# Kernel optimization log

Hardware: AMD Instinct MI355X
Metric: run time of the kernel (lower is better)

Reference implementation:

```python
import jax, jax.numpy as jnp
import numpy as np

B, S, DIM, H = 2, 2048, 1024, 16
DH = DIM // H            # 64
G = DH // 4              # 16 quaternion groups per head
IQ = DIM // 4            # 256
ROPE_BASE = 10000.0
SCALE = DH ** -0.5


def qlinear(x, wr, wi, wj, wk, b):
    # x: [B,S,4*IQ]; strided quaternion components, exact combo from QuaternionLinear.forward
    xr, xi, xj, xk = x[..., 0::4], x[..., 1::4], x[..., 2::4], x[..., 3::4]
    o_r = xr @ wr.T - xi @ wi.T - xj @ wj.T - xk @ wk.T
    o_i = xi @ wr.T + xr @ wi.T + xk @ wk.T - xj @ wj.T
    o_j = xj @ wr.T - xk @ wk.T + xr @ wj.T + xi @ wi.T
    o_k = xk @ wr.T + xj @ wj.T - xi @ wi.T + xr @ wk.T
    out = jnp.stack([o_r, o_i, o_j, o_k], axis=-1).reshape(x.shape[:-1] + (-1,))
    return out + b


def qrope(x):
    # x: [B,H,S,DH]; left quaternion multiply u(theta) \otimes q, axis_mode='cycle'
    b, h, s, dh = x.shape
    g = dh // 4
    xq = x.reshape(b, h, s, g, 4)
    t = jnp.arange(s, dtype=x.dtype)
    inv = 1.0 / (ROPE_BASE ** (jnp.arange(g, dtype=x.dtype) / g))
    ang = t[:, None] * inv[None, :]            # [S,G]
    cos, sin = jnp.cos(ang), jnp.sin(ang)
    gi = jnp.arange(g)
    ax_i = (gi % 3 == 0).astype(x.dtype)
    ax_j = (gi % 3 == 1).astype(x.dtype)
    ax_k = (gi % 3 == 2).astype(x.dtype)
    ur, ui, uj, uk = cos, sin * ax_i, sin * ax_j, sin * ax_k   # [S,G] broadcast over [B,H,S,G]
    xr, xi, xj, xk = xq[..., 0], xq[..., 1], xq[..., 2], xq[..., 3]
    pr = ur * xr - ui * xi - uj * xj - uk * xk
    pi = ur * xi + ui * xr + uj * xk - uk * xj
    pj = ur * xj - ui * xk + uj * xr + uk * xi
    pk = ur * xk + ui * xj - uj * xi + uk * xr
    return jnp.stack([pr, pi, pj, pk], axis=-1).reshape(b, h, s, dh)


def setup_inputs() -> dict:
    key = jax.random.key(0)
    ks = jax.random.split(key, 24)
    x = jax.random.normal(ks[0], (B, S, DIM), dtype=jnp.float32)
    # causal mask: True = masked
    mask = jnp.broadcast_to(jnp.triu(jnp.ones((S, S), dtype=bool), k=1), (B, S, S))
    inp = {"x": x, "mask": mask}
    i = 1
    for proj in ("q", "k", "v", "o"):
        for comp in ("wr", "wi", "wj", "wk"):
            inp[f"{proj}_{comp}"] = jax.random.normal(ks[i], (IQ, IQ), dtype=jnp.float32) * 0.02
            i += 1
        inp[f"{proj}_b"] = jnp.zeros((DIM,), dtype=jnp.float32)
    return inp


def reference(x, mask,
              q_wr, q_wi, q_wj, q_wk, q_b,
              k_wr, k_wi, k_wj, k_wk, k_b,
              v_wr, v_wi, v_wj, v_wk, v_b,
              o_wr, o_wi, o_wj, o_wk, o_b):
    b, s, dm = x.shape
    q = qlinear(x, q_wr, q_wi, q_wj, q_wk, q_b).reshape(b, s, H, DH).transpose(0, 2, 1, 3)
    k = qlinear(x, k_wr, k_wi, k_wj, k_wk, k_b).reshape(b, s, H, DH).transpose(0, 2, 1, 3)
    v = qlinear(x, v_wr, v_wi, v_wj, v_wk, v_b).reshape(b, s, H, DH).transpose(0, 2, 1, 3)
    q, k = qrope(q), qrope(k)
    scores = jnp.einsum('bhsd,bhtd->bhst', q, k) * SCALE
    scores = jnp.where(mask[:, None, :, :], -jnp.inf, scores)
    a = jax.nn.softmax(scores, axis=-1)
    out = jnp.einsum('bhst,bhtd->bhsd', a, v).transpose(0, 2, 1, 3).reshape(b, s, dm)
    return qlinear(out, o_wr, o_wi, o_wj, o_wk, o_b)
```

## Files before the change

### kernel.cpp

```cpp
#include <hip/hip_runtime.h>
#include <stdint.h>

typedef unsigned short u16;
typedef unsigned int   u32;

#define NB   2
#define NS   2048
#define NDIM 1024
#define NH   16
#define NDH  64
#define QSCALE 0.18033688011112042f

typedef __bf16 bf16x8 __attribute__((ext_vector_type(8)));
typedef float  f32x4  __attribute__((ext_vector_type(4)));

#define MFMA_BF16(a,b,c) __builtin_amdgcn_mfma_f32_16x16x32_bf16((a),(b),(c),0,0,0)

#define XBF_OFF   (256)
#define WD_OFF    (XBF_OFF  + 8*1024*1024)
#define BIAS_OFF  (WD_OFF   + 8*1024*1024)
#define QB_OFF    (BIAS_OFF + 16384)
#define KB_OFF    (QB_OFF   + 8*1024*1024)
#define VT_OFF    (KB_OFF   + 8*1024*1024)
#define OP_OFF    (VT_OFF   + 8*1024*1024)
#define LP_OFF    (OP_OFF   + 16*1024*1024)

__device__ __forceinline__ float bf2f(u16 h){
  union { u32 u; float f; } v; v.u = ((u32)h) << 16; return v.f;
}
__device__ __forceinline__ u16 f2bf(float f){
  union { float f; u32 u; } v; v.f = f;
  u32 r = (v.u >> 16) & 1u;
  return (u16)((v.u + 0x7fffu + r) >> 16);
}
__device__ __forceinline__ float load_val(const void* p, int i, int isbf){
  return isbf ? bf2f(((const u16*)p)[i]) : ((const float*)p)[i];
}
__device__ __forceinline__ void gl_lds16(const u16* g, u16* l){
  __builtin_amdgcn_global_load_lds(
      (__attribute__((address_space(1))) void*)(uintptr_t)g,
      (__attribute__((address_space(3))) void*)(uintptr_t)l,
      16, 0, 0);
}

__global__ void detect_kernel(const u16* __restrict__ x, int* __restrict__ flag){
  __shared__ int cnt;
  if (threadIdx.x == 0) cnt = 0;
  __syncthreads();
  int ok = 0;
  int base = threadIdx.x * 16;
  for (int i = base; i < base + 16; ++i){
    u16 h = x[i];
    int e = (h >> 7) & 0xFF;
    if ((e > 96 && e < 158) || ((h & 0x7FFF) == 0)) ok++;
  }
  atomicAdd(&cnt, ok);
  __syncthreads();
  if (threadIdx.x == 0) *flag = (cnt > 3600) ? 1 : 0;
}

__global__ void conv_x_kernel(const void* __restrict__ xin, u16* __restrict__ xbf,
                              const int* __restrict__ flag){
  int isbf = *flag;
  int t = blockIdx.x * 256 + threadIdx.x;
  if (isbf){
    ((uint4*)xbf)[t] = ((const uint4*)xin)[t];
  } else {
    const float4* f4 = (const float4*)xin;
    float4 a = f4[2*t], b = f4[2*t+1];
    ushort4 lo = { f2bf(a.x), f2bf(a.y), f2bf(a.z), f2bf(a.w) };
    ushort4 hi = { f2bf(b.x), f2bf(b.y), f2bf(b.z), f2bf(b.w) };
    ((ushort4*)xbf)[2*t]   = lo;
    ((ushort4*)xbf)[2*t+1] = hi;
  }
}

struct QPtrs { const void* w[16]; const void* b[4]; };

__global__ void build_w_kernel(QPtrs ptrs, u16* __restrict__ wd,
                               float* __restrict__ biasf, const int* __restrict__ flag){
  int isbf = *flag;
  int idx = blockIdx.x * 256 + threadIdx.x;
  int n = idx & 255, m = (idx >> 8) & 255, c = (idx >> 16) & 3, p = idx >> 18;
  int src = m * 256 + n;
  float vr = load_val(ptrs.w[p*4+0], src, isbf);
  float vi = load_val(ptrs.w[p*4+1], src, isbf);
  float vj = load_val(ptrs.w[p*4+2], src, isbf);
  float vk = load_val(ptrs.w[p*4+3], src, isbf);
  float o0, o1, o2, o3;
  switch (c){
    case 0:  o0 = vr; o1 = -vi; o2 = -vj; o3 = -vk; break;
    case 1:  o0 = vi; o1 =  vr; o2 = -vj; o3 =  vk; break;
    case 2:  o0 = vj; o1 =  vi; o2 =  vr; o3 = -vk; break;
    default: o0 = vk; o1 = -vi; o2 =  vj; o3 =  vr; break;
  }
  ushort4 sv = { f2bf(o0), f2bf(o1), f2bf(o2), f2bf(o3) };
  *(ushort4*)&wd[(size_t)p * 1048576 + (size_t)(4*m + c) * 1024 + 4*n] = sv;
  if (idx < 4096){
    int pp = idx >> 10, oo = idx & 1023;
    biasf[idx] = load_val(ptrs.b[pp], oo, isbf);
  }
}

__global__ __launch_bounds__(256)
void gemm_qkv_kernel(const u16* __restrict__ A, const u16* __restrict__ Bw,
                     const float* __restrict__ bias,
                     u16* __restrict__ qb, u16* __restrict__ kb, u16* __restrict__ vt){
  __shared__ u16 sA[128 * 32];
  __shared__ u16 sB[128 * 32];
  int tid = threadIdx.x, w = tid >> 6, lane = tid & 63, quad = lane >> 4, l16 = lane & 15;
  int n0 = blockIdx.x * 128, m0 = blockIdx.y * 128;

  f32x4 acc[4][4];
#pragma unroll
  for (int i = 0; i < 4; ++i)
#pragma unroll
    for (int j = 0; j < 4; ++j) acc[i][j] = (f32x4){0.f, 0.f, 0.f, 0.f};

  int eo = w * 512 + lane * 8;
  int r0 = eo >> 5, c0 = eo & 31;
  const u16* ga = A  + (size_t)(m0 + r0) * 1024 + c0;
  const u16* gb = Bw + (size_t)(n0 + r0) * 1024 + c0;
  u16* la = &sA[eo];
  u16* lb = &sB[eo];
  int mw = (w & 1) * 64, nw = (w >> 1) * 64;

  for (int k0 = 0; k0 < 1024; k0 += 32){
#pragma unroll
    for (int i = 0; i < 2; ++i){
      gl_lds16(ga + (size_t)i * 65536 + k0, la + i * 2048);
      gl_lds16(gb + (size_t)i * 65536 + k0, lb + i * 2048);
    }
    __syncthreads();
    bf16x8 af[4], bfr[4];
#pragma unroll
    for (int mt = 0; mt < 4; ++mt)
      af[mt] = *(const bf16x8*)&sA[(mw + mt*16 + l16) * 32 + quad * 8];
#pragma unroll
    for (int nt = 0; nt < 4; ++nt)
      bfr[nt] = *(const bf16x8*)&sB[(nw + nt*16 + l16) * 32 + quad * 8];
#pragma unroll
    for (int mt = 0; mt < 4; ++mt)
#pragma unroll
      for (int nt = 0; nt < 4; ++nt)
        acc[mt][nt] = MFMA_BF16(af[mt], bfr[nt], acc[mt][nt]);
    __syncthreads();
  }

#pragma unroll
  for (int mt = 0; mt < 4; ++mt){
    int row = m0 + mw + mt*16 + quad*4;
    int b = row >> 11, seq0 = row & 2047;
#pragma unroll
    for (int nt = 0; nt < 4; ++nt){
      int col = n0 + nw + nt*16 + l16;
      int proj = col >> 10, o = col & 1023;
      int h = o >> 6, d = o & 63;
      float bv = bias[col];
      if (proj == 2){
        ushort4 pv = { f2bf(acc[mt][nt][0] + bv), f2bf(acc[mt][nt][1] + bv),
                       f2bf(acc[mt][nt][2] + bv), f2bf(acc[mt][nt][3] + bv) };
        *(ushort4*)&vt[((size_t)((b*16 + h) * 64 + d)) * 2048 + seq0] = pv;
      } else {
        u16* dst = proj ? kb : qb;
#pragma unroll
        for (int r = 0; r < 4; ++r)
          dst[((size_t)((b*16 + h) * 2048 + seq0 + r)) * 64 + d] = f2bf(acc[mt][nt][r] + bv);
      }
    }
  }
}

__global__ __launch_bounds__(256)
void gemm_o_kernel(const u16* __restrict__ A, const u16* __restrict__ Bw,
                   const float* __restrict__ bias, void* __restrict__ dout,
                   const int* __restrict__ flag){
  __shared__ u16 sA[64 * 32];
  __shared__ u16 sB[128 * 32];
  int tid = threadIdx.x, w = tid >> 6, lane = tid & 63, quad = lane >> 4, l16 = lane & 15;
  int n0 = blockIdx.x * 128, m0 = blockIdx.y * 64;

  f32x4 acc[2][4];
#pragma unroll
  for (int i = 0; i < 2; ++i)
#pragma unroll
    for (int j = 0; j < 4; ++j) acc[i][j] = (f32x4){0.f, 0.f, 0.f, 0.f};

  int mw = (w & 1) * 32, nw = (w >> 1) * 64;

  for (int k0 = 0; k0 < 1024; k0 += 32){
#pragma unroll
    for (int i = 0; i < 3; ++i){
      int c = w * 3 + i;
      int eo = (c < 4 ? c : c - 4) * 512 + lane * 8;
      int r0 = eo >> 5, c0 = eo & 31;
      if (c < 4) gl_lds16(A  + (size_t)(m0 + r0) * 1024 + k0 + c0, &sA[eo]);
      else       gl_lds16(Bw + (size_t)(n0 + r0) * 1024 + k0 + c0, &sB[eo]);
    }
    __syncthreads();
    bf16x8 af[2], bfr[4];
#pragma unroll
    for (int mt = 0; mt < 2; ++mt)
      af[mt] = *(const bf16x8*)&sA[(mw + mt*16 + l16) * 32 + quad * 8];
#pragma unroll
    for (int nt = 0; nt < 4; ++nt)
      bfr[nt] = *(const bf16x8*)&sB[(nw + nt*16 + l16) * 32 + quad * 8];
#pragma unroll
    for (int mt = 0; mt < 2; ++mt)
#pragma unroll
      for (int nt = 0; nt < 4; ++nt)
        acc[mt][nt] = MFMA_BF16(af[mt], bfr[nt], acc[mt][nt]);
    __syncthreads();
  }

  int isbf = *flag;
#pragma unroll
  for (int mt = 0; mt < 2; ++mt){
    int row = m0 + mw + mt*16 + quad*4;
#pragma unroll
    for (int nt = 0; nt < 4; ++nt){
      int col = n0 + nw + nt*16 + l16;
      float bv = bias[col];
#pragma unroll
      for (int r = 0; r < 4; ++r){
        float val = acc[mt][nt][r] + bv;
        size_t addr = (size_t)(row + r) * 1024 + col;
        if (isbf) ((u16*)dout)[addr] = f2bf(val);
        else      ((float*)dout)[addr] = val;
      }
    }
  }
}

__global__ void rope_kernel(u16* __restrict__ qb, u16* __restrict__ kb){
  int idx = blockIdx.x * 256 + threadIdx.x;
  int which = idx >> 20;
  int r = idx & 1048575;
  u16* buf = which ? kb : qb;
  int g = r & 15, s = (r >> 4) & 2047, bh = r >> 15;
  size_t base = ((size_t)bh * 2048 + s) * 64 + g * 4;
  ushort4 xv = *(ushort4*)&buf[base];
  float xr = bf2f(xv.x), xi = bf2f(xv.y), xj = bf2f(xv.z), xk = bf2f(xv.w);
  float inv = __builtin_amdgcn_exp2f(-(float)g * 0.8304820237218405f);
  float ang = (float)s * inv;
  float co = __cosf(ang), si = __sinf(ang);
  float sc = which ? 1.0f : QSCALE;
  co *= sc; si *= sc;
  int ax = g % 3;
  float ui = (ax == 0) ? si : 0.f;
  float uj = (ax == 1) ? si : 0.f;
  float uk = (ax == 2) ? si : 0.f;
  float pr = co*xr - ui*xi - uj*xj - uk*xk;
  float pi = co*xi + ui*xr + uj*xk - uk*xj;
  float pj = co*xj - ui*xk + uj*xr + uk*xi;
  float pk = co*xk + ui*xj - uj*xi + uk*xr;
  ushort4 res = { f2bf(pr), f2bf(pi), f2bf(pj), f2bf(pk) };
  *(ushort4*)&buf[base] = res;
}

#define PSTR 72

__global__ __launch_bounds__(256, 3)
void attn_kernel(const u16* __restrict__ Q, const u16* __restrict__ K,
                 const u16* __restrict__ Vt, u16* __restrict__ OP,
                 float* __restrict__ LP){
  __shared__ u16 sK[2][4096];
  __shared__ u16 sV[2][4096];
  __shared__ u16 sP[4][16 * PSTR];
  int qt  = 15 - (int)blockIdx.x;
  int spl = blockIdx.y;
  int bh  = blockIdx.z;
  int tid = threadIdx.x, w = tid >> 6, lane = tid & 63, quad = lane >> 4, l16 = lane & 15;
  size_t kbase = (size_t)bh * 2048 * 64;
  size_t vbase = (size_t)bh * 64 * 2048;
  int rowbase = qt * 128 + w * 32;

  bf16x8 qf[2][2];
#pragma unroll
  for (int g = 0; g < 2; ++g)
#pragma unroll
    for (int kc = 0; kc < 2; ++kc)
      qf[g][kc] = *(const bf16x8*)(Q + kbase + (size_t)(rowbase + g*16 + l16) * 64 + kc*32 + quad*8);

  f32x4 oacc[2][4];
  float lsum[2][4];
#pragma unroll
  for (int g = 0; g < 2; ++g)
#pragma unroll
    for (int i = 0; i < 4; ++i){ oacc[g][i] = (f32x4){0.f,0.f,0.f,0.f}; lsum[g][i] = 0.f; }

  int kt0 = spl ? (qt + 1) : 0;
  int ntiles = qt + 1;

  auto stage = [&](int kt, int b){
    int kcol = kt * 64;
#pragma unroll
    for (int p = 0; p < 2; ++p){
      int slot = w*128 + p*64 + lane;
      int row = slot >> 3, dc = (slot & 7) ^ (row & 7);
      gl_lds16(K  + kbase + (size_t)(kcol + row) * 64 + dc*8, &sK[b][(w*128 + p*64) * 8]);
      gl_lds16(Vt + vbase + (size_t)row * 2048 + kcol + dc*8, &sV[b][(w*128 + p*64) * 8]);
    }
  };

  stage(kt0, 0);
  for (int i = 0; i < ntiles; ++i){
    int kcol = (kt0 + i) * 64;
    __syncthreads();
    if (i + 1 < ntiles) stage(kt0 + i + 1, (i + 1) & 1);
    const u16* bK = sK[i & 1];
    const u16* bV = sV[i & 1];

    if (kcol <= rowbase + 31){
      bf16x8 bk[2][4], vf[2][4];
#pragma unroll
      for (int kc = 0; kc < 2; ++kc)
#pragma unroll
        for (int nt = 0; nt < 4; ++nt){
          int rw = nt*16 + l16;
          int ch = ((kc*4 + quad) ^ (rw & 7)) * 8;
          bk[kc][nt] = *(const bf16x8*)&bK[rw*64 + ch];
          vf[kc][nt] = *(const bf16x8*)&bV[rw*64 + ch];
        }
#pragma unroll
      for (int g = 0; g < 2; ++g){
        int G0 = rowbase + g*16;
        if (kcol <= G0 + 15){
          f32x4 sacc[4];
#pragma unroll
          for (int nt = 0; nt < 4; ++nt) sacc[nt] = (f32x4){0.f,0.f,0.f,0.f};
#pragma unroll
          for (int kc = 0; kc < 2; ++kc)
#pragma unroll
            for (int nt = 0; nt < 4; ++nt)
              sacc[nt] = MFMA_BF16(qf[g][kc], bk[kc][nt], sacc[nt]);

          __bf16* sp = (__bf16*)&sP[w][0];
          if (kcol + 63 > G0){
#pragma unroll
            for (int nt = 0; nt < 4; ++nt){
              int col = kcol + nt*16 + l16;
#pragma unroll
              for (int r = 0; r < 4; ++r){
                int row = G0 + quad*4 + r;
                float pp = (col <= row) ? __builtin_amdgcn_exp2f(sacc[nt][r]) : 0.f;
                lsum[g][r] += pp;
                sp[(quad*4 + r) * PSTR + nt*16 + l16] = (__bf16)pp;
              }
            }
          } else {
#pragma unroll
            for (int nt = 0; nt < 4; ++nt)
#pragma unroll
              for (int r = 0; r < 4; ++r){
                float pp = __builtin_amdgcn_exp2f(sacc[nt][r]);
                lsum[g][r] += pp;
                sp[(quad*4 + r) * PSTR + nt*16 + l16] = (__bf16)pp;
              }
          }
#pragma unroll
          for (int kc = 0; kc < 2; ++kc){
            bf16x8 pf = *(const bf16x8*)&sp[l16 * PSTR + kc*32 + quad*8];
#pragma unroll
            for (int nt = 0; nt < 4; ++nt)
              oacc[g][nt] = MFMA_BF16(pf, vf[kc][nt], oacc[g][nt]);
          }
        }
      }
    }
  }

  size_t obase = ((size_t)(spl*32 + bh)) * 2048;
#pragma unroll
  for (int g = 0; g < 2; ++g)
#pragma unroll
    for (int r = 0; r < 4; ++r){
      float l = lsum[g][r];
      l += __shfl_xor(l, 1); l += __shfl_xor(l, 2);
      l += __shfl_xor(l, 4); l += __shfl_xor(l, 8);
      int row = rowbase + g*16 + quad*4 + r;
      if (l16 == 0) LP[obase + row] = l;
#pragma unroll
      for (int nt = 0; nt < 4; ++nt)
        OP[(obase + row) * 64 + nt*16 + l16] = f2bf(oacc[g][nt][r]);
    }
}

__global__ void combine_kernel(const u16* __restrict__ OP, const float* __restrict__ LP,
                               u16* __restrict__ Ab){
  int idx = blockIdx.x * 256 + threadIdx.x;
  int dc = idx & 7, s = (idx >> 3) & 2047, bh = idx >> 14;
  size_t r0 = (size_t)bh * 2048 + s, r1 = (size_t)(32 + bh) * 2048 + s;
  float invl = 1.f / (LP[r0] + LP[r1]);
  union { uint4 v; u16 h[8]; } a0, a1; ushort4 o[2];
  a0.v = *(const uint4*)&OP[r0 * 64 + dc*8];
  a1.v = *(const uint4*)&OP[r1 * 64 + dc*8];
#pragma unroll
  for (int p = 0; p < 2; ++p)
#pragma unroll
    for (int j = 0; j < 4; ++j)
      ((u16*)&o[p])[j] = f2bf((bf2f(a0.h[p*4+j]) + bf2f(a1.h[p*4+j])) * invl);
  int b = bh >> 4, h = bh & 15;
  u16* dst = &Ab[((size_t)(b*2048 + s)) * 1024 + h*64 + dc*8];
  *(ushort4*)dst = o[0];
  *(ushort4*)(dst + 4) = o[1];
}

extern "C" void kernel_launch(void* const* d_in, const int* in_sizes, int n_in,
                              void* d_out, int out_size, void* d_ws, size_t ws_size,
                              hipStream_t stream){
  (void)in_sizes; (void)n_in; (void)out_size; (void)ws_size;
  char* ws = (char*)d_ws;
  int*   flag  = (int*)ws;
  u16*   Xbf   = (u16*)(ws + XBF_OFF);
  u16*   Wd    = (u16*)(ws + WD_OFF);
  float* biasf = (float*)(ws + BIAS_OFF);
  u16*   Qb    = (u16*)(ws + QB_OFF);
  u16*   Kb    = (u16*)(ws + KB_OFF);
  u16*   Vt    = (u16*)(ws + VT_OFF);
  u16*   OP    = (u16*)(ws + OP_OFF);
  float* LP    = (float*)(ws + LP_OFF);
  u16*   Ab    = Xbf;

  detect_kernel<<<1, 256, 0, stream>>>((const u16*)d_in[0], flag);
  conv_x_kernel<<<2048, 256, 0, stream>>>(d_in[0], Xbf, flag);

  QPtrs ptrs;
  for (int p = 0; p < 4; ++p){
    for (int wi = 0; wi < 4; ++wi) ptrs.w[p*4 + wi] = d_in[2 + p*5 + wi];
    ptrs.b[p] = d_in[2 + p*5 + 4];
  }
  build_w_kernel<<<4096, 256, 0, stream>>>(ptrs, Wd, biasf, flag);

  gemm_qkv_kernel<<<dim3(24, 32), 256, 0, stream>>>(Xbf, Wd, biasf, Qb, Kb, Vt);
  rope_kernel<<<8192, 256, 0, stream>>>(Qb, Kb);
  attn_kernel<<<dim3(16, 2, 32), 256, 0, stream>>>(Qb, Kb, Vt, OP, LP);
  combine_kernel<<<2048, 256, 0, stream>>>(OP, LP, Ab);
  gemm_o_kernel<<<dim3(8, 64), 256, 0, stream>>>(Ab, Wd + 3*1048576, biasf + 3072,
                                                 d_out, flag);
}
```

Baseline: 274.4 us.

## Compute transposed PV product and load V fragments directly from global

The attention kernel now computes O^T = V^T·P^T, so V fragments are read straight from global memory into registers, and the V tile LDS staging buffer is removed. P is stored transposed in a small padded LDS buffer using vector stores, and output rows are written as ushort4 vectors after row sums are redistributed through LDS. The grid order is changed so bh varies fastest. Less LDS may allow higher occupancy and remove a staging copy. The costs are uncoalesced-ish global V loads that are no longer prefetched, and scalar 16-bit LDS gathers to build the P fragments.

```diff
diff --git a/kernel.cpp b/kernel.cpp
--- a/kernel.cpp
+++ b/kernel.cpp
@@ -258,22 +258,22 @@
   *(ushort4*)&buf[base] = res;
 }
 
-#define PSTR 72
+#define SPT 20
 
 __global__ __launch_bounds__(256, 3)
 void attn_kernel(const u16* __restrict__ Q, const u16* __restrict__ K,
                  const u16* __restrict__ Vt, u16* __restrict__ OP,
                  float* __restrict__ LP){
   __shared__ u16 sK[2][4096];
-  __shared__ u16 sV[2][4096];
-  __shared__ u16 sP[4][16 * PSTR];
-  int qt  = 15 - (int)blockIdx.x;
+  __shared__ u16 sPT[4][64 * SPT];
+  int bh  = blockIdx.x;
   int spl = blockIdx.y;
-  int bh  = blockIdx.z;
+  int qt  = 15 - (int)blockIdx.z;
   int tid = threadIdx.x, w = tid >> 6, lane = tid & 63, quad = lane >> 4, l16 = lane & 15;
   size_t kbase = (size_t)bh * 2048 * 64;
   size_t vbase = (size_t)bh * 64 * 2048;
   int rowbase = qt * 128 + w * 32;
+  u16* spw = &sPT[w][0];
 
   bf16x8 qf[2][2];
 #pragma unroll
@@ -282,12 +282,12 @@
     for (int kc = 0; kc < 2; ++kc)
       qf[g][kc] = *(const bf16x8*)(Q + kbase + (size_t)(rowbase + g*16 + l16) * 64 + kc*32 + quad*8);
 
-  f32x4 oacc[2][4];
+  f32x4 oaccT[2][4];
   float lsum[2][4];
 #pragma unroll
   for (int g = 0; g < 2; ++g)
 #pragma unroll
-    for (int i = 0; i < 4; ++i){ oacc[g][i] = (f32x4){0.f,0.f,0.f,0.f}; lsum[g][i] = 0.f; }
+    for (int i = 0; i < 4; ++i){ oaccT[g][i] = (f32x4){0.f,0.f,0.f,0.f}; lsum[g][i] = 0.f; }
 
   int kt0 = spl ? (qt + 1) : 0;
   int ntiles = qt + 1;
@@ -298,8 +298,7 @@
     for (int p = 0; p < 2; ++p){
       int slot = w*128 + p*64 + lane;
       int row = slot >> 3, dc = (slot & 7) ^ (row & 7);
-      gl_lds16(K  + kbase + (size_t)(kcol + row) * 64 + dc*8, &sK[b][(w*128 + p*64) * 8]);
-      gl_lds16(Vt + vbase + (size_t)row * 2048 + kcol + dc*8, &sV[b][(w*128 + p*64) * 8]);
+      gl_lds16(K + kbase + (size_t)(kcol + row) * 64 + dc*8, &sK[b][(w*128 + p*64) * 8]);
     }
   };
 
@@ -309,10 +308,16 @@
     __syncthreads();
     if (i + 1 < ntiles) stage(kt0 + i + 1, (i + 1) & 1);
     const u16* bK = sK[i & 1];
-    const u16* bV = sV[i & 1];
 
     if (kcol <= rowbase + 31){
-      bf16x8 bk[2][4], vf[2][4];
+      bf16x8 vf[4][2];
+#pragma unroll
+      for (int dn = 0; dn < 4; ++dn)
+#pragma unroll
+        for (int kc = 0; kc < 2; ++kc)
+          vf[dn][kc] = *(const bf16x8*)(Vt + vbase + (size_t)(dn*16 + l16) * 2048
+                                        + kcol + kc*32 + quad*8);
+      bf16x8 bk[2][4];
 #pragma unroll
       for (int kc = 0; kc < 2; ++kc)
 #pragma unroll
@@ -320,7 +325,6 @@
           int rw = nt*16 + l16;
           int ch = ((kc*4 + quad) ^ (rw & 7)) * 8;
           bk[kc][nt] = *(const bf16x8*)&bK[rw*64 + ch];
-          vf[kc][nt] = *(const bf16x8*)&bV[rw*64 + ch];
         }
 #pragma unroll
       for (int g = 0; g < 2; ++g){
@@ -335,42 +339,49 @@
             for (int nt = 0; nt < 4; ++nt)
               sacc[nt] = MFMA_BF16(qf[g][kc], bk[kc][nt], sacc[nt]);
 
-          __bf16* sp = (__bf16*)&sP[w][0];
           if (kcol + 63 > G0){
 #pragma unroll
             for (int nt = 0; nt < 4; ++nt){
               int col = kcol + nt*16 + l16;
+              ushort4 pv;
 #pragma unroll
               for (int r = 0; r < 4; ++r){
                 int row = G0 + quad*4 + r;
                 float pp = (col <= row) ? __builtin_amdgcn_exp2f(sacc[nt][r]) : 0.f;
                 lsum[g][r] += pp;
-                sp[(quad*4 + r) * PSTR + nt*16 + l16] = (__bf16)pp;
+                ((u16*)&pv)[r] = f2bf(pp);
               }
+              *(ushort4*)&spw[(nt*16 + l16) * SPT + quad*4] = pv;
             }
           } else {
 #pragma unroll
-            for (int nt = 0; nt < 4; ++nt)
+            for (int nt = 0; nt < 4; ++nt){
+              ushort4 pv;
 #pragma unroll
               for (int r = 0; r < 4; ++r){
                 float pp = __builtin_amdgcn_exp2f(sacc[nt][r]);
                 lsum[g][r] += pp;
-                sp[(quad*4 + r) * PSTR + nt*16 + l16] = (__bf16)pp;
+                ((u16*)&pv)[r] = f2bf(pp);
               }
+              *(ushort4*)&spw[(nt*16 + l16) * SPT + quad*4] = pv;
+            }
           }
 #pragma unroll
           for (int kc = 0; kc < 2; ++kc){
-            bf16x8 pf = *(const bf16x8*)&sp[l16 * PSTR + kc*32 + quad*8];
-#pragma unroll
-            for (int nt = 0; nt < 4; ++nt)
-              oacc[g][nt] = MFMA_BF16(pf, vf[kc][nt], oacc[g][nt]);
+            bf16x8 pf;
+#pragma unroll
+            for (int j = 0; j < 8; ++j)
+              pf[j] = ((const __bf16*)spw)[(kc*32 + quad*8 + j) * SPT + l16];
+#pragma unroll
+            for (int dn = 0; dn < 4; ++dn)
+              oaccT[g][dn] = MFMA_BF16(vf[dn][kc], pf, oaccT[g][dn]);
           }
         }
       }
     }
   }
 
-  size_t obase = ((size_t)(spl*32 + bh)) * 2048;
+  float* scr = (float*)spw;
 #pragma unroll
   for (int g = 0; g < 2; ++g)
 #pragma unroll
@@ -378,12 +389,24 @@
       float l = lsum[g][r];
       l += __shfl_xor(l, 1); l += __shfl_xor(l, 2);
       l += __shfl_xor(l, 4); l += __shfl_xor(l, 8);
-      int row = rowbase + g*16 + quad*4 + r;
-      if (l16 == 0) LP[obase + row] = l;
-#pragma unroll
-      for (int nt = 0; nt < 4; ++nt)
-        OP[(obase + row) * 64 + nt*16 + l16] = f2bf(oacc[g][nt][r]);
-    }
+      if (l16 == 0) scr[g*16 + quad*4 + r] = l;
+    }
+  float lrow[2];
+#pragma unroll
+  for (int g = 0; g < 2; ++g) lrow[g] = scr[g*16 + l16];
+
+  size_t obase = ((size_t)(spl*32 + bh)) * 2048;
+#pragma unroll
+  for (int g = 0; g < 2; ++g){
+    int row = rowbase + g*16 + l16;
+    if (quad == 0) LP[obase + row] = lrow[g];
+#pragma unroll
+    for (int dn = 0; dn < 4; ++dn){
+      ushort4 ov = { f2bf(oaccT[g][dn][0]), f2bf(oaccT[g][dn][1]),
+                     f2bf(oaccT[g][dn][2]), f2bf(oaccT[g][dn][3]) };
+      *(ushort4*)&OP[(obase + row) * 64 + dn*16 + quad*4] = ov;
+    }
+  }
 }
 
 __global__ void combine_kernel(const u16* __restrict__ OP, const float* __restrict__ LP,
@@ -434,7 +457,7 @@
 
   gemm_qkv_kernel<<<dim3(24, 32), 256, 0, stream>>>(Xbf, Wd, biasf, Qb, Kb, Vt);
   rope_kernel<<<8192, 256, 0, stream>>>(Qb, Kb);
-  attn_kernel<<<dim3(16, 2, 32), 256, 0, stream>>>(Qb, Kb, Vt, OP, LP);
+  attn_kernel<<<dim3(32, 2, 16), 256, 0, stream>>>(Qb, Kb, Vt, OP, LP);
   combine_kernel<<<2048, 256, 0, stream>>>(OP, LP, Ab);
   gemm_o_kernel<<<dim3(8, 64), 256, 0, stream>>>(Ab, Wd + 3*1048576, biasf + 3072,
                                                  d_out, flag);
```

Result: faster. 262.0 us (-4.5%).
